# Kernel optimization log

Measured on AMD Instinct MI355X. Metric: run time of the kernel, lower is better.

The kernel has to match this reference:

```python
import jax, jax.numpy as jnp
import numpy as np

BATCH, T, N_STATES, EMIT = 128, 8192, 128, 64


def setup_inputs() -> dict:
    key = jax.random.key(0)
    kobs, kI, kA, kB = jax.random.split(key, 4)
    # one-hot observation sequences, as fed to the RNN cell
    obs = jax.random.randint(kobs, (BATCH, T), 0, EMIT)
    inputs = jax.nn.one_hot(obs, EMIT, dtype=jnp.float32)  # [B, T, EMIT]
    # valid probability parameters (model.I/A/B produce normalized matrices)
    I = jax.nn.softmax(jax.random.normal(kI, (N_STATES,), dtype=jnp.float32))
    A = jax.nn.softmax(jax.random.normal(kA, (N_STATES, N_STATES), dtype=jnp.float32), axis=-1)
    B = jax.nn.softmax(jax.random.normal(kB, (EMIT, N_STATES), dtype=jnp.float32), axis=0)
    return {"inputs": inputs, "I": I, "A": A, "B": B}


def reference(inputs, I, A, B):
    # HMM scaled forward algorithm, exactly the CgpHmmCell.call math,
    # run over the sequence with lax.scan (what keras.layers.RNN does step-wise).
    x = jnp.swapaxes(inputs, 0, 1)  # [T, batch, EMIT]

    # t == 0 (count == 1): R = I, Z = 1
    E0 = x[0] @ B                               # [batch, S]
    alpha0 = E0 * I[None, :]                    # [batch, S]
    loglik0 = jnp.log(jnp.sum(alpha0, axis=-1, keepdims=True))  # [batch, 1]

    def step(carry, x_t):
        alpha, loglik = carry
        Z = jnp.sum(alpha, axis=-1, keepdims=True)      # Z_{i-1}
        R = (alpha / Z) @ A                             # scaled forward @ A
        E = x_t @ B                                     # emission probs
        alpha_new = E * R
        loglik_new = loglik + jnp.log(jnp.sum(alpha_new, axis=-1, keepdims=True))
        return (alpha_new, loglik_new), None

    (alpha_f, loglik_f), _ = jax.lax.scan(step, (alpha0, loglik0), x[1:])
    return alpha_f, loglik_f
```

## Files before the change

kernel.cpp:

```cpp
#include <hip/hip_runtime.h>


#define BATCH 128
#define TLEN 8192
#define NS 128
#define EMIT 64
#define NCHUNK 256
#define CLEN (TLEN / NCHUNK)
#define WARM 8
#define BG 8
#define BSTR 132
#define LN64 4.158883083359672f

typedef __attribute__((ext_vector_type(8))) short short8;
typedef __attribute__((ext_vector_type(4))) float floatx4;
typedef __attribute__((ext_vector_type(4))) unsigned int uintx4;

__device__ __forceinline__ unsigned f2bf(float f) {
    return (__float_as_uint(f) + 0x8000u) >> 16;
}

__global__ __launch_bounds__(256) void decode_onehot(
        const floatx4* __restrict__ x, unsigned char* __restrict__ obsG,
        float* __restrict__ out_ll) {
    if (blockIdx.x == 0 && threadIdx.x < BATCH) out_ll[threadIdx.x] = 0.f;
    int base = blockIdx.x * 512 + threadIdx.x;
    #pragma unroll
    for (int h = 0; h < 2; ++h) {
        int i = base + h * 256;
        floatx4 v = __builtin_nontemporal_load(&x[i]);
        float s = v.x + v.y + v.z + v.w;
        if (s > 0.5f) {
            int e = (v.y > 0.5f) ? 1 : (v.z > 0.5f) ? 2 : (v.w > 0.5f) ? 3 : 0;
            int elem = (i << 2) + e;
            int row = elem >> 6;
            int col = elem & 63;
            int b = row >> 13;
            int t = row & (TLEN - 1);
            obsG[(b >> 4) * (16 * TLEN) + (b & 15) * TLEN + t] = (unsigned char)col;
        }
    }
}

__global__ __launch_bounds__(64) void hmm_scan(
        const float* __restrict__ Amat,
        const float* __restrict__ Bmat,
        const float* __restrict__ Ivec,
        const unsigned char* __restrict__ obsG,
        float* __restrict__ out_alpha,
        float* __restrict__ out_ll)
{
    __shared__ unsigned short Bl[EMIT * BSTR];

    const int lane = threadIdx.x;
    const int n = lane & 15;
    const int q = lane >> 4;
    const int bg = blockIdx.x >> 8;
    const int c = blockIdx.x & (NCHUNK - 1);
    const bool first = (c == 0);
    const bool lastc = (c == NCHUNK - 1);
    const int steps = first ? CLEN : (CLEN + WARM);
    const int t0 = first ? 0 : c * CLEN - WARM;

    for (int i = lane; i < EMIT * NS; i += 64) {
        int e = i >> 7, col = i & (NS - 1);
        Bl[e * BSTR + col] = (unsigned short)f2bf(64.0f * Bmat[i]);
    }

    const unsigned char* orow = obsG + bg * (16 * TLEN) + n * TLEN;
    unsigned ow[10];
    if (first) {
        uintx4 a = *(const uintx4*)(orow);
        uintx4 b = *(const uintx4*)(orow + 16);
        ow[0] = a.x; ow[1] = a.y; ow[2] = a.z; ow[3] = a.w;
        ow[4] = b.x; ow[5] = b.y; ow[6] = b.z; ow[7] = b.w;
        ow[8] = 0; ow[9] = 0;
    } else {
        uint2 a = *(const uint2*)(orow + t0);
        uintx4 b = *(const uintx4*)(orow + t0 + 8);
        uintx4 d = *(const uintx4*)(orow + t0 + 24);
        ow[0] = a.x; ow[1] = a.y;
        ow[2] = b.x; ow[3] = b.y; ow[4] = b.z; ow[5] = b.w;
        ow[6] = d.x; ow[7] = d.y; ow[8] = d.z; ow[9] = d.w;
    }

    short8 af[8][4];
    #pragma unroll
    for (int mt = 0; mt < 8; ++mt)
        #pragma unroll
        for (int kf = 0; kf < 4; ++kf) {
            short8 v;
            #pragma unroll
            for (int j = 0; j < 8; ++j) {
                int u = 32 * kf + 8 * q + j;
                int sk = 32 * (u >> 5) + 16 * ((u >> 2) & 1)
                       + 4 * ((u >> 3) & 3) + (u & 3);
                v[j] = (short)f2bf(Amat[sk * NS + 16 * mt + n]);
            }
            af[mt][kf] = v;
        }
    __syncthreads();

    unsigned pk[16];
    #pragma unroll
    for (int i = 0; i < 16; ++i) pk[i] = 0x3C003C00u;

    float s_pre = 1.0f, s_penult = 1.0f, s_end = 1.0f;

    for (int it = 0; it < steps; ++it) {
        floatx4 acc[8];
        if (first && it == 0) {
            #pragma unroll
            for (int mt = 0; mt < 8; ++mt)
                acc[mt] = *(const floatx4*)(Ivec + 16 * mt + 4 * q);
        } else {
            short8 bf[4];
            #pragma unroll
            for (int kf = 0; kf < 4; ++kf) {
                uintx4 u4 = {pk[4 * kf], pk[4 * kf + 1], pk[4 * kf + 2], pk[4 * kf + 3]};
                bf[kf] = __builtin_bit_cast(short8, u4);
            }
            #pragma unroll
            for (int mt = 0; mt < 8; ++mt) {
                floatx4 a = {0.f, 0.f, 0.f, 0.f};
                #pragma unroll
                for (int kf = 0; kf < 4; ++kf)
                    a = __builtin_amdgcn_mfma_f32_16x16x32_bf16(af[mt][kf], bf[kf], a, 0, 0, 0);
                acc[mt] = a;
            }
        }

        int o = (ow[it >> 2] >> ((it & 3) * 8)) & 0xFF;
        int eb = o * BSTR;
        #pragma unroll
        for (int mt = 0; mt < 8; ++mt) {
            const unsigned* ep = (const unsigned*)(Bl + eb + 16 * mt + 4 * q);
            unsigned d0 = ep[0], d1 = ep[1];
            acc[mt].x *= __uint_as_float(d0 << 16);
            acc[mt].y *= __uint_as_float(d0 & 0xFFFF0000u);
            acc[mt].z *= __uint_as_float(d1 << 16);
            acc[mt].w *= __uint_as_float(d1 & 0xFFFF0000u);
        }

        bool need_red = (it == steps - 1) || (!first && it == WARM - 1) ||
                        (lastc && it == steps - 2);
        if (need_red) {
            float zz = 0.f;
            #pragma unroll
            for (int mt = 0; mt < 8; ++mt)
                zz += (acc[mt].x + acc[mt].y) + (acc[mt].z + acc[mt].w);
            zz += __shfl_xor(zz, 16, 64);
            zz += __shfl_xor(zz, 32, 64);
            if (it == steps - 1) s_end = zz;
            else if (lastc && it == steps - 2) s_penult = zz;
            else s_pre = zz;
        }

        if (lastc && it == steps - 1) {
            float inv = 1.0f / (64.0f * s_penult);
            #pragma unroll
            for (int mt = 0; mt < 8; ++mt) {
                floatx4 o4;
                o4.x = acc[mt].x * inv; o4.y = acc[mt].y * inv;
                o4.z = acc[mt].z * inv; o4.w = acc[mt].w * inv;
                *(floatx4*)(out_alpha + (bg * 16 + n) * NS + 16 * mt + 4 * q) = o4;
            }
        }

        #pragma unroll
        for (int mt = 0; mt < 8; ++mt) {
            unsigned u0 = __float_as_uint(acc[mt].x) + 0x8000u;
            unsigned u1 = __float_as_uint(acc[mt].y) + 0x8000u;
            unsigned u2 = __float_as_uint(acc[mt].z) + 0x8000u;
            unsigned u3 = __float_as_uint(acc[mt].w) + 0x8000u;
            pk[2 * mt]     = __builtin_amdgcn_perm(u1, u0, 0x07060302u);
            pk[2 * mt + 1] = __builtin_amdgcn_perm(u3, u2, 0x07060302u);
        }
    }

    if (q == 0) {
        float ll = __logf(s_end) - __logf(s_pre) - (float)CLEN * LN64;
        atomicAdd(&out_ll[bg * 16 + n], ll);
    }
}

extern "C" void kernel_launch(void* const* d_in, const int* in_sizes, int n_in,
                              void* d_out, int out_size, void* d_ws, size_t ws_size,
                              hipStream_t stream) {
    const float* x = (const float*)d_in[0];
    const float* I = (const float*)d_in[1];
    const float* A = (const float*)d_in[2];
    const float* B = (const float*)d_in[3];
    float* out = (float*)d_out;

    unsigned char* obsG = (unsigned char*)d_ws;

    decode_onehot<<<(BATCH * TLEN * 16) / 512, 256, 0, stream>>>(
        (const floatx4*)x, obsG, out + BATCH * NS);
    hmm_scan<<<BG * NCHUNK, 64, 0, stream>>>(A, B, I, obsG, out, out + BATCH * NS);
}
```

Measured before the change: 389.3 us.

## Fuse one-hot decoding into the HMM scan kernel via wave ballots

Drops the separate decode kernel and its byte-index workspace. Each scan block now reads the one-hot rows for its own chunk, including the warm-up overlap, straight from the input. It decodes them with wave ballots into a small shared-memory index table, and a tiny kernel zeroes the log-likelihood output. This removes a kernel launch and the write and re-read of the intermediate index array. In exchange, about a quarter more of the one-hot input is read because warm-up windows overlap, and the 16-row decode loop runs serially inside small blocks, which may be latency-bound.

```diff
diff --git a/kernel.cpp b/kernel.cpp
--- a/kernel.cpp
+++ b/kernel.cpp
@@ -10,6 +10,7 @@
 #define WARM 8
 #define BG 8
 #define BSTR 132
+#define OSTR 48
 #define LN64 4.158883083359672f
 
 typedef __attribute__((ext_vector_type(8))) short short8;
@@ -20,37 +21,20 @@
     return (__float_as_uint(f) + 0x8000u) >> 16;
 }
 
-__global__ __launch_bounds__(256) void decode_onehot(
-        const floatx4* __restrict__ x, unsigned char* __restrict__ obsG,
-        float* __restrict__ out_ll) {
-    if (blockIdx.x == 0 && threadIdx.x < BATCH) out_ll[threadIdx.x] = 0.f;
-    int base = blockIdx.x * 512 + threadIdx.x;
-    #pragma unroll
-    for (int h = 0; h < 2; ++h) {
-        int i = base + h * 256;
-        floatx4 v = __builtin_nontemporal_load(&x[i]);
-        float s = v.x + v.y + v.z + v.w;
-        if (s > 0.5f) {
-            int e = (v.y > 0.5f) ? 1 : (v.z > 0.5f) ? 2 : (v.w > 0.5f) ? 3 : 0;
-            int elem = (i << 2) + e;
-            int row = elem >> 6;
-            int col = elem & 63;
-            int b = row >> 13;
-            int t = row & (TLEN - 1);
-            obsG[(b >> 4) * (16 * TLEN) + (b & 15) * TLEN + t] = (unsigned char)col;
-        }
-    }
+__global__ void zero_ll(float* __restrict__ out_ll) {
+    out_ll[threadIdx.x] = 0.f;
 }
 
 __global__ __launch_bounds__(64) void hmm_scan(
+        const floatx4* __restrict__ x,
         const float* __restrict__ Amat,
         const float* __restrict__ Bmat,
         const float* __restrict__ Ivec,
-        const unsigned char* __restrict__ obsG,
         float* __restrict__ out_alpha,
         float* __restrict__ out_ll)
 {
     __shared__ unsigned short Bl[EMIT * BSTR];
+    __shared__ unsigned char obs_l[16 * OSTR];
 
     const int lane = threadIdx.x;
     const int n = lane & 15;
@@ -67,21 +51,37 @@
         Bl[e * BSTR + col] = (unsigned short)f2bf(64.0f * Bmat[i]);
     }
 
-    const unsigned char* orow = obsG + bg * (16 * TLEN) + n * TLEN;
-    unsigned ow[10];
-    if (first) {
-        uintx4 a = *(const uintx4*)(orow);
-        uintx4 b = *(const uintx4*)(orow + 16);
-        ow[0] = a.x; ow[1] = a.y; ow[2] = a.z; ow[3] = a.w;
-        ow[4] = b.x; ow[5] = b.y; ow[6] = b.z; ow[7] = b.w;
-        ow[8] = 0; ow[9] = 0;
-    } else {
-        uint2 a = *(const uint2*)(orow + t0);
-        uintx4 b = *(const uintx4*)(orow + t0 + 8);
-        uintx4 d = *(const uintx4*)(orow + t0 + 24);
-        ow[0] = a.x; ow[1] = a.y;
-        ow[2] = b.x; ow[3] = b.y; ow[4] = b.z; ow[5] = b.w;
-        ow[6] = d.x; ow[7] = d.y; ow[8] = d.z; ow[9] = d.w;
+    {
+        const int p_local = lane >> 4;
+        const int jj = lane & 15;
+        for (int bl = 0; bl < 16; ++bl) {
+            const floatx4* bp = x + (((bg * 16 + bl) * TLEN + t0 + p_local) << 4) + jj;
+            floatx4 vv[10];
+            #pragma unroll
+            for (int tg = 0; tg < 10; ++tg) vv[tg] = bp[tg * 64];
+            #pragma unroll
+            for (int tg = 0; tg < 10; ++tg) {
+                floatx4 v = vv[tg];
+                bool found = (v.x > 0.5f) || (v.y > 0.5f) || (v.z > 0.5f) || (v.w > 0.5f);
+                bool e1 = (v.y > 0.5f) || (v.w > 0.5f);
+                bool e2 = (v.z > 0.5f) || (v.w > 0.5f);
+                unsigned long long m1 = __ballot(found);
+                unsigned long long m2 = __ballot(e1);
+                unsigned long long m3 = __ballot(e2);
+                unsigned packed = 0;
+                #pragma unroll
+                for (int p = 0; p < 4; ++p) {
+                    unsigned g = (unsigned)(m1 >> (16 * p)) & 0xFFFFu;
+                    int j16 = __builtin_ctz(g);
+                    int bit = 16 * p + j16;
+                    unsigned e = (unsigned)((m2 >> bit) & 1ull) |
+                                 ((unsigned)((m3 >> bit) & 1ull) << 1);
+                    packed |= (unsigned)(j16 * 4 + e) << (8 * p);
+                }
+                if (lane == 0)
+                    *(unsigned*)(obs_l + bl * OSTR + tg * 4) = packed;
+            }
+        }
     }
 
     short8 af[8][4];
@@ -100,6 +100,16 @@
             af[mt][kf] = v;
         }
     __syncthreads();
+
+    unsigned ow[10];
+    {
+        uintx4 wa = *(const uintx4*)(obs_l + n * OSTR);
+        uintx4 wb = *(const uintx4*)(obs_l + n * OSTR + 16);
+        uint2  wc = *(const uint2*)(obs_l + n * OSTR + 32);
+        ow[0] = wa.x; ow[1] = wa.y; ow[2] = wa.z; ow[3] = wa.w;
+        ow[4] = wb.x; ow[5] = wb.y; ow[6] = wb.z; ow[7] = wb.w;
+        ow[8] = wc.x; ow[9] = wc.y;
+    }
 
     unsigned pk[16];
     #pragma unroll
@@ -193,9 +203,7 @@
     const float* B = (const float*)d_in[3];
     float* out = (float*)d_out;
 
-    unsigned char* obsG = (unsigned char*)d_ws;
-
-    decode_onehot<<<(BATCH * TLEN * 16) / 512, 256, 0, stream>>>(
-        (const floatx4*)x, obsG, out + BATCH * NS);
-    hmm_scan<<<BG * NCHUNK, 64, 0, stream>>>(A, B, I, obsG, out, out + BATCH * NS);
-}
+    zero_ll<<<1, BATCH, 0, stream>>>(out + BATCH * NS);
+    hmm_scan<<<BG * NCHUNK, 64, 0, stream>>>(
+        (const floatx4*)x, A, B, I, out, out + BATCH * NS);
+}
```

Result: slower. 411.8 us (+5.8%).
